# Kernel optimization log

Measured on AMD Instinct MI355X. Metric: run time of the kernel, lower is better.

## Reference

```python
import jax, jax.numpy as jnp
import numpy as np

H = 16
ATTN_TEMP = 1.5
CLS_TEMP = 2.0


def setup_inputs() -> dict:
    key = jax.random.key(0)
    ks = jax.random.split(key, 11)
    B, Nq, Nk, C = 2, 2048, 2048, 1024
    x_q = jax.random.normal(ks[0], (B, Nq, C), jnp.float32)
    x_kv = jax.random.normal(ks[1], (B, Nk, C), jnp.float32)
    cls_token = jax.random.normal(ks[2], (B, 1, C), jnp.float32)
    s = 0.02
    Wq = jax.random.normal(ks[3], (C, C), jnp.float32) * s
    bq = jax.random.normal(ks[4], (C,), jnp.float32) * s
    Wk = jax.random.normal(ks[5], (C, C), jnp.float32) * s
    bk = jax.random.normal(ks[6], (C,), jnp.float32) * s
    Wv = jax.random.normal(ks[7], (C, C), jnp.float32) * s
    bv = jax.random.normal(ks[8], (C,), jnp.float32) * s
    Wp = jax.random.normal(ks[9], (C, C), jnp.float32) * s
    bp = jax.random.normal(ks[10], (C,), jnp.float32) * s
    return {"x_q": x_q, "x_kv": x_kv, "cls_token": cls_token,
            "Wq": Wq, "bq": bq, "Wk": Wk, "bk": bk, "Wv": Wv, "bv": bv,
            "Wp": Wp, "bp": bp}


def reference(x_q, x_kv, cls_token, Wq, bq, Wk, bk, Wv, bv, Wp, bp):
    B, Nq, C = x_q.shape
    Nk = x_kv.shape[1]
    Dh = C // H
    scale = Dh ** -0.5
    # torch Linear: y = x @ W.T + b, W is [out, in]
    q = (x_q @ Wq.T + bq).reshape(B, Nq, H, Dh).transpose(0, 2, 1, 3)   # [B,H,Nq,Dh]
    k = (x_kv @ Wk.T + bk).reshape(B, Nk, H, Dh).transpose(0, 2, 1, 3)  # [B,H,Nk,Dh]
    v = (x_kv @ Wv.T + bv).reshape(B, Nk, H, Dh).transpose(0, 2, 1, 3)  # [B,H,Nk,Dh]
    attn_logits = jnp.einsum('bhqd,bhkd->bhqk', q, k) * (scale / ATTN_TEMP)
    # cls-token affinity mask: raw cls_token (NOT passed through q-proj)
    cls_tok = cls_token.reshape(B, 1, H, Dh).transpose(0, 2, 1, 3)      # [B,H,1,Dh]
    aff = jax.nn.sigmoid(jnp.einsum('bhqd,bhkd->bhqk', cls_tok, k) * (scale / CLS_TEMP))
    aff = aff.mean(axis=1, keepdims=True)                               # [B,1,1,Nk]
    m = aff.min(axis=-1, keepdims=True)
    M = aff.max(axis=-1, keepdims=True)
    aff_mask = (aff - m) / (M - m + 1e-6)
    attn = jax.nn.softmax(attn_logits, axis=-1) * aff_mask              # [B,H,Nq,Nk]
    x = jnp.einsum('bhqk,bhkd->bqhd', attn, v).reshape(B, Nq, C)
    x = x @ Wp.T + bp
    return (x, attn_logits.sum(axis=1) / H, aff_mask)
```

## Files before the change

kernel.cpp:

```cpp
#include <hip/hip_runtime.h>
#include <stdint.h>
#include <math.h>

typedef unsigned short u16;
typedef __attribute__((ext_vector_type(8))) short bh8;
typedef __attribute__((ext_vector_type(4))) float f32x4;
typedef __attribute__((ext_vector_type(16))) float f32x16;

#define MFMA16(a,b,c) __builtin_amdgcn_mfma_f32_16x16x32_bf16((a),(b),(c),0,0,0)
#define MFMA32(a,b,c) __builtin_amdgcn_mfma_f32_32x32x16_bf16((a),(b),(c),0,0,0)

__device__ __forceinline__ int swz3(int r){ return (r ^ (r >> 3)) & 7; }

__device__ __forceinline__ u16 f2bf(float f){
  union { float f; uint32_t i; } x; x.f = f;
  uint32_t r = x.i + 0x7fffu + ((x.i >> 16) & 1u);
  return (u16)(r >> 16);
}
__device__ __forceinline__ float bf2f(u16 u){
  union { uint32_t i; float f; } x; x.i = ((uint32_t)u) << 16; return x.f;
}
__device__ __forceinline__ uint32_t cvtpk(float a, float b){
  uint32_t r;
  asm("v_cvt_pk_bf16_f32 %0, %1, %2" : "=v"(r) : "v"(a), "v"(b));
  return r;
}

__device__ __forceinline__ void gld16(void* lds, const void* g){
  __builtin_amdgcn_global_load_lds(
      (__attribute__((address_space(1))) unsigned int*)const_cast<void*>(g),
      (__attribute__((address_space(3))) unsigned int*)lds, 16, 0, 0);
}

__global__ __launch_bounds__(256) void cvt_all_kernel(
    const float* __restrict__ xq, const float* __restrict__ xkv,
    const float* __restrict__ Wq, const float* __restrict__ Wk,
    const float* __restrict__ Wv, const float* __restrict__ Wp,
    u16* __restrict__ oxq, u16* __restrict__ oxkv,
    u16* __restrict__ oWq, u16* __restrict__ oWk,
    u16* __restrict__ oWv, u16* __restrict__ oWp,
    int nx8, int nw8)
{
  int i = blockIdx.x * 256 + threadIdx.x;
  const float* s; u16* d; int o;
  if (i < 2 * nx8){
    if (i < nx8){ s = xq; d = oxq; o = i; }
    else        { s = xkv; d = oxkv; o = i - nx8; }
  } else {
    int k = i - 2 * nx8;
    if (k >= 4 * nw8) return;
    int wsel = k / nw8; o = k - wsel * nw8;
    s = (wsel == 0) ? Wq : (wsel == 1) ? Wk : (wsel == 2) ? Wv : Wp;
    d = (wsel == 0) ? oWq : (wsel == 1) ? oWk : (wsel == 2) ? oWv : oWp;
  }
  const float4* sp = (const float4*)s + 2 * (size_t)o;
  float4 a = sp[0], b = sp[1];
  bh8 r;
  r[0]=(short)f2bf(a.x); r[1]=(short)f2bf(a.y); r[2]=(short)f2bf(a.z); r[3]=(short)f2bf(a.w);
  r[4]=(short)f2bf(b.x); r[5]=(short)f2bf(b.y); r[6]=(short)f2bf(b.z); r[7]=(short)f2bf(b.w);
  *(bh8*)(d + (size_t)o * 8) = r;
}

template<bool OUT_BF16, bool HAS_BIAS>
__device__ __forceinline__ void gemm_body(
    const u16* __restrict__ A, const u16* __restrict__ Bm,
    const float* __restrict__ bias, void* __restrict__ outp,
    int N, int K, int bm, int bn, float scale,
    u16* As, u16* Bs)
{
  const int tid = threadIdx.x, lane = tid & 63, w = tid >> 6;
  const int wm = w >> 1, wn = w & 1;
  const int l15 = lane & 15, l4 = lane >> 4;
  f32x4 acc[4][4];
  const f32x4 vz = {0.f, 0.f, 0.f, 0.f};
  #pragma unroll
  for (int m = 0; m < 4; ++m)
    #pragma unroll
    for (int n = 0; n < 4; ++n) acc[m][n] = vz;

  const u16* Arow = A + (size_t)bm * K;
  const u16* Brow = Bm + (size_t)bn * K;
  const int nkt = K >> 6;
  for (int kt = 0; kt < nkt; ++kt){
    #pragma unroll
    for (int it = 0; it < 4; ++it){
      int cb = w * 256 + it * 64;
      int c = cb + lane;
      int j = c >> 3;
      int dd = (c & 7) ^ swz3(j);
      gld16(&As[cb * 8], Arow + (size_t)j * K + kt * 64 + dd * 8);
      gld16(&Bs[cb * 8], Brow + (size_t)j * K + kt * 64 + dd * 8);
    }
    __syncthreads();
    #pragma unroll
    for (int s = 0; s < 2; ++s){
      bh8 af[4], bfr[4];
      #pragma unroll
      for (int m = 0; m < 4; ++m){
        int row = wm * 64 + m * 16 + l15;
        af[m] = *(const bh8*)&As[row * 64 + (((s * 4 + l4) ^ swz3(row)) << 3)];
      }
      #pragma unroll
      for (int n = 0; n < 4; ++n){
        int row = wn * 64 + n * 16 + l15;
        bfr[n] = *(const bh8*)&Bs[row * 64 + (((s * 4 + l4) ^ swz3(row)) << 3)];
      }
      #pragma unroll
      for (int m = 0; m < 4; ++m)
        #pragma unroll
        for (int n = 0; n < 4; ++n)
          acc[m][n] = MFMA16(af[m], bfr[n], acc[m][n]);
    }
    __syncthreads();
  }
  #pragma unroll
  for (int m = 0; m < 4; ++m){
    int row0 = bm + wm * 64 + m * 16 + l4 * 4;
    #pragma unroll
    for (int n = 0; n < 4; ++n){
      int col = bn + wn * 64 + n * 16 + l15;
      float bv = HAS_BIAS ? bias[col] : 0.f;
      #pragma unroll
      for (int r = 0; r < 4; ++r){
        float v = (acc[m][n][r] + bv) * scale;
        size_t idx = (size_t)(row0 + r) * N + col;
        if (OUT_BF16) ((u16*)outp)[idx] = f2bf(v);
        else          ((float*)outp)[idx] = v;
      }
    }
  }
}

__global__ __launch_bounds__(256) void proj_gemm_kernel(
    const u16* __restrict__ xq, const u16* __restrict__ xkv,
    const u16* __restrict__ Wq, const u16* __restrict__ Wk, const u16* __restrict__ Wv,
    const float* __restrict__ bq, const float* __restrict__ bk, const float* __restrict__ bv,
    u16* __restrict__ Q, u16* __restrict__ Ko, u16* __restrict__ V, float qscale)
{
  __shared__ __align__(16) u16 As[128 * 64];
  __shared__ __align__(16) u16 Bs[128 * 64];
  int z = blockIdx.z;
  const u16* A   = (z == 0) ? xq : xkv;
  const u16* W   = (z == 0) ? Wq : (z == 1) ? Wk : Wv;
  const float* b = (z == 0) ? bq : (z == 1) ? bk : bv;
  u16* out       = (z == 0) ? Q  : (z == 1) ? Ko : V;
  float sc       = (z == 0) ? qscale : 1.0f;
  gemm_body<true, true>(A, W, b, out, 1024, 1024,
                        blockIdx.y * 128, blockIdx.x * 128, sc, As, Bs);
}

__global__ __launch_bounds__(256) void out1_gemm_kernel(
    const u16* __restrict__ Q, const u16* __restrict__ Kb,
    float* __restrict__ out1, int Nq, int Nk, float scale)
{
  __shared__ __align__(16) u16 As[128 * 64];
  __shared__ __align__(16) u16 Bs[128 * 64];
  int b = blockIdx.z;
  gemm_body<false, false>(Q + (size_t)b * Nq * 1024, Kb + (size_t)b * Nk * 1024,
                          nullptr, out1 + (size_t)b * Nq * Nk, Nk, 1024,
                          blockIdx.y * 128, blockIdx.x * 128, scale, As, Bs);
}

__global__ __launch_bounds__(256) void out0_gemm_kernel(
    const u16* __restrict__ X, const u16* __restrict__ Wp,
    const float* __restrict__ bp, float* __restrict__ out)
{
  __shared__ __align__(16) u16 As[128 * 64];
  __shared__ __align__(16) u16 Bs[128 * 64];
  gemm_body<false, true>(X, Wp, bp, out, 1024, 1024,
                         blockIdx.y * 128, blockIdx.x * 128, 1.0f, As, Bs);
}

__global__ __launch_bounds__(256) void aff_kernel(
    const float* __restrict__ cls, const u16* __restrict__ Kb,
    float* __restrict__ aff, int Nk)
{
  int lane = threadIdx.x & 63;
  int gw = (blockIdx.x * 256 + threadIdx.x) >> 6;
  int b = gw / Nk, j = gw - b * Nk;
  const u16* kr = Kb + ((size_t)(b * Nk + j)) * 1024;
  const float* c = cls + (size_t)b * 1024;
  float total = 0.f;
  #pragma unroll
  for (int half = 0; half < 2; ++half){
    int d0 = half * 512 + lane * 8;
    bh8 kv = *(const bh8*)(kr + d0);
    float4 ca = *(const float4*)(c + d0);
    float4 cb = *(const float4*)(c + d0 + 4);
    float p = bf2f((u16)kv[0]) * ca.x + bf2f((u16)kv[1]) * ca.y
            + bf2f((u16)kv[2]) * ca.z + bf2f((u16)kv[3]) * ca.w
            + bf2f((u16)kv[4]) * cb.x + bf2f((u16)kv[5]) * cb.y
            + bf2f((u16)kv[6]) * cb.z + bf2f((u16)kv[7]) * cb.w;
    p += __shfl_xor(p, 1); p += __shfl_xor(p, 2); p += __shfl_xor(p, 4);
    float sig = 1.f / (1.f + __expf(-0.0625f * p));
    total += sig;
  }
  total += __shfl_xor(total, 8); total += __shfl_xor(total, 16); total += __shfl_xor(total, 32);
  if (lane == 0) aff[gw] = total * (1.0f / 128.0f);
}

__global__ __launch_bounds__(1024) void affnorm_kernel(
    const float* __restrict__ aff, float* __restrict__ mask,
    float* __restrict__ out2, int Nk)
{
  int b = blockIdx.x, tid = threadIdx.x;
  const float* a = aff + (size_t)b * Nk;
  float mn = 1e30f, mx = -1e30f;
  for (int i = tid; i < Nk; i += 1024){
    float v = a[i]; mn = fminf(mn, v); mx = fmaxf(mx, v);
  }
  #pragma unroll
  for (int off = 1; off < 64; off <<= 1){
    mn = fminf(mn, __shfl_xor(mn, off));
    mx = fmaxf(mx, __shfl_xor(mx, off));
  }
  __shared__ float smn[16], smx[16];
  int wv = tid >> 6;
  if ((tid & 63) == 0){ smn[wv] = mn; smx[wv] = mx; }
  __syncthreads();
  mn = smn[tid & 15]; mx = smx[tid & 15];
  #pragma unroll
  for (int off = 1; off < 16; off <<= 1){
    mn = fminf(mn, __shfl_xor(mn, off));
    mx = fmaxf(mx, __shfl_xor(mx, off));
  }
  float inv = 1.f / ((mx - mn) + 1e-6f);
  for (int i = tid; i < Nk; i += 1024){
    float v = (a[i] - mn) * inv;
    mask[(size_t)b * Nk + i] = v;
    out2[(size_t)b * Nk + i] = v;
  }
}

__global__ __launch_bounds__(256) void vtrans_kernel(
    const u16* __restrict__ Vb, const float* __restrict__ affm,
    u16* __restrict__ Vtg, int Nk)
{
  __shared__ u16 T[64][72];
  int t0 = blockIdx.x * 64, h = blockIdx.y, b = blockIdx.z;
  int tid = threadIdx.x;
  int row = tid & 63, cp = tid >> 6;
  const u16* src = Vb + ((size_t)(b * Nk) + t0 + row) * 1024 + h * 64 + cp * 16;
  *(bh8*)&T[row][cp * 16]     = *(const bh8*)(src);
  *(bh8*)&T[row][cp * 16 + 8] = *(const bh8*)(src + 8);
  __syncthreads();
  int d = tid >> 2, kc = (tid & 3) * 16;
  const float* av = affm + (size_t)b * Nk + t0 + kc;
  u16* dst = Vtg + ((size_t)(b * 16 + h) * 64 + d) * 2048 + t0 + kc;
  bh8 o0, o1;
  #pragma unroll
  for (int j = 0; j < 8; ++j)
    o0[j] = (short)f2bf(bf2f(T[kc + j][d]) * av[j]);
  #pragma unroll
  for (int j = 0; j < 8; ++j)
    o1[j] = (short)f2bf(bf2f(T[kc + 8 + j][d]) * av[8 + j]);
  *(bh8*)dst = o0;
  *(bh8*)(dst + 8) = o1;
}

__global__ __launch_bounds__(256) void flash_kernel(
    const u16* __restrict__ Qb, const u16* __restrict__ Kb, const u16* __restrict__ Vtg,
    u16* __restrict__ xo, int Nq, int Nk, int nqb, int perx)
{
  __shared__ __align__(16) u16 Ks[2][64 * 64];
  __shared__ __align__(16) u16 Vs[2][64 * 64];
  const int tid = threadIdx.x, lane = tid & 63, w = tid >> 6;
  const int l31 = lane & 31, hi = lane >> 5;

  int bid = blockIdx.x;
  int xcd = bid & 7, slot = bid >> 3;
  int g = xcd * perx + slot / nqb;
  int qb = slot - (slot / nqb) * nqb;
  int h = g & 15, b = g >> 4;
  int q0 = qb * 128;

  const u16* Qg = Qb + ((size_t)b * Nq + q0 + w * 32 + l31) * 1024 + h * 64;
  const u16* Kg = Kb + ((size_t)b * Nk) * 1024 + h * 64;
  const u16* Vg = Vtg + ((size_t)(b * 16 + h)) * 64 * 2048;

  bh8 qf[4];
  #pragma unroll
  for (int s = 0; s < 4; ++s)
    qf[s] = *(const bh8*)(Qg + s * 16 + hi * 8);

  float lsum = 0.f;
  f32x16 O0, O1;
  #pragma unroll
  for (int r = 0; r < 16; ++r){ O0[r] = 0.f; O1[r] = 0.f; }

  const int nt = Nk >> 6;

  #define STAGE(T, PB) do {                                                    \
    int t_ = (T);                                                              \
    _Pragma("unroll")                                                          \
    for (int it = 0; it < 2; ++it){                                            \
      int cb = (w * 2 + it) * 64;                                              \
      int c = cb + lane;                                                       \
      int j = c >> 3, dd = (c & 7) ^ swz3(j);                                  \
      gld16(&Ks[PB][cb * 8], Kg + (size_t)(t_ * 64 + j) * 1024 + dd * 8);      \
      gld16(&Vs[PB][cb * 8], Vg + (size_t)j * 2048 + t_ * 64 + dd * 8);        \
    }                                                                          \
  } while (0)

  STAGE(0, 0);
  __syncthreads();

  for (int t = 0; t < nt; ++t){
    int pb = t & 1;
    if (t + 1 < nt) STAGE(t + 1, pb ^ 1);

    f32x16 S0, S1;
    #pragma unroll
    for (int s = 0; s < 4; ++s){
      bh8 kf0 = *(const bh8*)&Ks[pb][l31 * 64 + (((s * 2 + hi) ^ swz3(l31)) << 3)];
      bh8 kf1 = *(const bh8*)&Ks[pb][(32 + l31) * 64 + (((s * 2 + hi) ^ swz3(32 + l31)) << 3)];
      if (s == 0){
        f32x16 z;
        #pragma unroll
        for (int r = 0; r < 16; ++r) z[r] = 0.f;
        S0 = MFMA32(kf0, qf[0], z);
        S1 = MFMA32(kf1, qf[0], z);
      } else {
        S0 = MFMA32(kf0, qf[s], S0);
        S1 = MFMA32(kf1, qf[s], S1);
      }
    }

    #pragma unroll
    for (int r = 0; r < 16; ++r) S0[r] = exp2f(S0[r]);
    #pragma unroll
    for (int r = 0; r < 16; ++r) S1[r] = exp2f(S1[r]);
    float rs = 0.f;
    #pragma unroll
    for (int r = 0; r < 16; ++r) rs += S0[r];
    #pragma unroll
    for (int r = 0; r < 16; ++r) rs += S1[r];
    rs += __shfl_xor(rs, 32);
    lsum += rs;

    bh8 pa[4];
    #pragma unroll
    for (int ks = 0; ks < 4; ++ks){
      int r0 = (ks & 1) * 8;
      float p0, p1, p2, p3, p4, p5, p6, p7;
      if (ks < 2){ p0=S0[r0]; p1=S0[r0+1]; p2=S0[r0+2]; p3=S0[r0+3];
                   p4=S0[r0+4]; p5=S0[r0+5]; p6=S0[r0+6]; p7=S0[r0+7]; }
      else       { p0=S1[r0]; p1=S1[r0+1]; p2=S1[r0+2]; p3=S1[r0+3];
                   p4=S1[r0+4]; p5=S1[r0+5]; p6=S1[r0+6]; p7=S1[r0+7]; }
      uint32_t x0 = cvtpk(p0, p1), x1 = cvtpk(p2, p3);
      uint32_t y0 = cvtpk(p4, p5), y1 = cvtpk(p6, p7);
      asm volatile("v_permlane32_swap_b32 %0, %1" : "+v"(x0), "+v"(y0));
      asm volatile("v_permlane32_swap_b32 %0, %1" : "+v"(x1), "+v"(y1));
      union { uint32_t u[4]; bh8 v; } pk;
      pk.u[0] = x0; pk.u[1] = x1; pk.u[2] = y0; pk.u[3] = y1;
      pa[ks] = pk.v;
    }

    #pragma unroll
    for (int ks = 0; ks < 4; ++ks){
      bh8 vf0 = *(const bh8*)&Vs[pb][l31 * 64 + (((ks * 2 + hi) ^ swz3(l31)) << 3)];
      bh8 vf1 = *(const bh8*)&Vs[pb][(32 + l31) * 64 + (((ks * 2 + hi) ^ swz3(32 + l31)) << 3)];
      O0 = MFMA32(pa[ks], vf0, O0);
      O1 = MFMA32(pa[ks], vf1, O1);
    }
    __syncthreads();
  }
  #undef STAGE

  float inv = 1.0f / lsum;
  int hb = hi << 4;
  #pragma unroll
  for (int r = 0; r < 16; ++r){
    int qc = (r & 3) + 8 * (r >> 2);
    float invq = __int_as_float(__builtin_amdgcn_ds_bpermute(qc * 4 + hb, __float_as_int(inv)));
    int qrow = q0 + w * 32 + qc + 4 * hi;
    size_t base = ((size_t)b * Nq + qrow) * 1024 + h * 64;
    xo[base + l31]      = f2bf(O0[r] * invq);
    xo[base + 32 + l31] = f2bf(O1[r] * invq);
  }
}

extern "C" void kernel_launch(void* const* d_in, const int* in_sizes, int n_in,
                              void* d_out, int out_size, void* d_ws, size_t ws_size,
                              hipStream_t stream)
{
  const float* x_q  = (const float*)d_in[0];
  const float* x_kv = (const float*)d_in[1];
  const float* cls  = (const float*)d_in[2];
  const float* bq   = (const float*)d_in[4];
  const float* bk   = (const float*)d_in[6];
  const float* bv   = (const float*)d_in[8];
  const float* bp   = (const float*)d_in[10];
  const float* Wq   = (const float*)d_in[3];
  const float* Wk   = (const float*)d_in[5];
  const float* Wv   = (const float*)d_in[7];
  const float* Wp   = (const float*)d_in[9];

  const int Nq = 2048, Nk = 2048, C = 1024;
  const int B = in_sizes[0] / (Nq * C);
  const size_t nX = (size_t)B * Nq * C;
  const size_t nW = (size_t)C * C;

  char* wsb = (char*)d_ws;
  size_t off = 0;
  auto alloc = [&](size_t bytes) -> char* {
    char* p = wsb + off; off += (bytes + 255) & ~(size_t)255; return p;
  };
  u16* xqb  = (u16*)alloc(nX * 2);
  u16* xkvb = (u16*)alloc(nX * 2);
  u16* Wqb  = (u16*)alloc(nW * 2);
  u16* Wkb  = (u16*)alloc(nW * 2);
  u16* Wvb  = (u16*)alloc(nW * 2);
  u16* Wpb  = (u16*)alloc(nW * 2);
  u16* Qb   = (u16*)alloc(nX * 2);
  u16* Kb   = (u16*)alloc(nX * 2);
  u16* Vb   = (u16*)alloc(nX * 2);
  u16* Vtg  = (u16*)alloc(nX * 2);
  u16* Xat  = (u16*)alloc(nX * 2);
  float* aff  = (float*)alloc((size_t)B * Nk * 4);
  float* affm = (float*)alloc((size_t)B * Nk * 4);

  float* out0 = (float*)d_out;
  float* out1 = out0 + (size_t)B * Nq * C;
  float* out2 = out1 + (size_t)B * Nq * Nk;

  int nx8 = (int)(nX / 8), nw8 = (int)(nW / 8);
  int total = 2 * nx8 + 4 * nw8;
  cvt_all_kernel<<<(total + 255) / 256, 256, 0, stream>>>(
      x_q, x_kv, Wq, Wk, Wv, Wp, xqb, xkvb, Wqb, Wkb, Wvb, Wpb, nx8, nw8);

  const float c2 = (0.125f / 1.5f) * 1.44269504088896f;
  proj_gemm_kernel<<<dim3(C / 128, (B * Nq) / 128, 3), 256, 0, stream>>>(
      xqb, xkvb, Wqb, Wkb, Wvb, bq, bk, bv, Qb, Kb, Vb, c2);

  aff_kernel<<<(B * Nk) / 4, 256, 0, stream>>>(cls, Kb, aff, Nk);
  affnorm_kernel<<<B, 1024, 0, stream>>>(aff, affm, out2, Nk);

  vtrans_kernel<<<dim3(Nk / 64, 16, B), 256, 0, stream>>>(Vb, affm, Vtg, Nk);

  const float c1s = (0.125f / (1.5f * 16.f)) / c2;
  out1_gemm_kernel<<<dim3(Nk / 128, Nq / 128, B), 256, 0, stream>>>(
      Qb, Kb, out1, Nq, Nk, c1s);

  int nqb = Nq / 128;
  int perx = (16 * B) / 8;
  flash_kernel<<<dim3(nqb * 16 * B), 256, 0, stream>>>(
      Qb, Kb, Vtg, Xat, Nq, Nk, nqb, perx);

  out0_gemm_kernel<<<dim3(C / 128, (B * Nq) / 128, 1), 256, 0, stream>>>(
      Xat, Wpb, bp, out0);
}
```

Before: 281.6 us.

## Split flash attention over key halves and merge partials in combine kernel

Splits the flash attention key range into two halves per query block, doubling the grid, and adds a combine kernel that sums the two partial outputs and normalizes by the summed row denominators. The row-sum reduction now runs as an extra MFMA against a ones vector instead of VALU adds plus a shuffle, and exp2f is replaced with a raw v_exp_f32 instruction. It also sets launch_bounds occupancy to 4 and reuses dead workspace buffers for the partials. The goal is more parallelism and less VALU work, at the cost of extra partial-result traffic in bf16 and an additional kernel launch.

```diff
diff --git a/kernel.cpp b/kernel.cpp
--- a/kernel.cpp
+++ b/kernel.cpp
@@ -24,6 +24,9 @@
   uint32_t r;
   asm("v_cvt_pk_bf16_f32 %0, %1, %2" : "=v"(r) : "v"(a), "v"(b));
   return r;
+}
+__device__ __forceinline__ float fexp2(float x){
+  float r; asm("v_exp_f32 %0, %1" : "=v"(r) : "v"(x)); return r;
 }
 
 __device__ __forceinline__ void gld16(void* lds, const void* g){
@@ -258,9 +261,9 @@
   *(bh8*)(dst + 8) = o1;
 }
 
-__global__ __launch_bounds__(256) void flash_kernel(
+__global__ __launch_bounds__(256, 4) void flash_kernel(
     const u16* __restrict__ Qb, const u16* __restrict__ Kb, const u16* __restrict__ Vtg,
-    u16* __restrict__ xo, int Nq, int Nk, int nqb, int perx)
+    u16* __restrict__ Opart, float* __restrict__ Lpart, int Nq, int Nk, int nqb, int perx)
 {
   __shared__ __align__(16) u16 Ks[2][64 * 64];
   __shared__ __align__(16) u16 Vs[2][64 * 64];
@@ -269,26 +272,37 @@
 
   int bid = blockIdx.x;
   int xcd = bid & 7, slot = bid >> 3;
-  int g = xcd * perx + slot / nqb;
-  int qb = slot - (slot / nqb) * nqb;
+  int spg = nqb * 2;
+  int gl = slot / spg;
+  int within = slot - gl * spg;
+  int g = xcd * perx + gl;
+  int qb = within >> 1, sp = within & 1;
   int h = g & 15, b = g >> 4;
   int q0 = qb * 128;
 
   const u16* Qg = Qb + ((size_t)b * Nq + q0 + w * 32 + l31) * 1024 + h * 64;
   const u16* Kg = Kb + ((size_t)b * Nk) * 1024 + h * 64;
-  const u16* Vg = Vtg + ((size_t)(b * 16 + h)) * 64 * 2048;
+  const u16* Vg = Vtg + ((size_t)(b * 16 + h)) * 64 * (size_t)Nk;
 
   bh8 qf[4];
   #pragma unroll
   for (int s = 0; s < 4; ++s)
     qf[s] = *(const bh8*)(Qg + s * 16 + hi * 8);
 
-  float lsum = 0.f;
-  f32x16 O0, O1;
-  #pragma unroll
-  for (int r = 0; r < 16; ++r){ O0[r] = 0.f; O1[r] = 0.f; }
-
-  const int nt = Nk >> 6;
+  union { short s[8]; bh8 v; } one8;
+  #pragma unroll
+  for (int j = 0; j < 8; ++j) one8.s[j] = (short)0x3F80;
+  const bh8 onesf = one8.v;
+
+  f32x16 O0, O1, Lacc;
+  #pragma unroll
+  for (int r = 0; r < 16; ++r){ O0[r] = 0.f; O1[r] = 0.f; Lacc[r] = 0.f; }
+  f32x16 z16;
+  #pragma unroll
+  for (int r = 0; r < 16; ++r) z16[r] = 0.f;
+
+  const int tpers = (Nk >> 6) >> 1;
+  const int t0 = sp * tpers;
 
   #define STAGE(T, PB) do {                                                    \
     int t_ = (T);                                                              \
@@ -298,16 +312,16 @@
       int c = cb + lane;                                                       \
       int j = c >> 3, dd = (c & 7) ^ swz3(j);                                  \
       gld16(&Ks[PB][cb * 8], Kg + (size_t)(t_ * 64 + j) * 1024 + dd * 8);      \
-      gld16(&Vs[PB][cb * 8], Vg + (size_t)j * 2048 + t_ * 64 + dd * 8);        \
+      gld16(&Vs[PB][cb * 8], Vg + (size_t)j * Nk + t_ * 64 + dd * 8);          \
     }                                                                          \
   } while (0)
 
-  STAGE(0, 0);
+  STAGE(t0, 0);
   __syncthreads();
 
-  for (int t = 0; t < nt; ++t){
-    int pb = t & 1;
-    if (t + 1 < nt) STAGE(t + 1, pb ^ 1);
+  for (int ti = 0; ti < tpers; ++ti){
+    int pb = ti & 1;
+    if (ti + 1 < tpers) STAGE(t0 + ti + 1, pb ^ 1);
 
     f32x16 S0, S1;
     #pragma unroll
@@ -315,11 +329,8 @@
       bh8 kf0 = *(const bh8*)&Ks[pb][l31 * 64 + (((s * 2 + hi) ^ swz3(l31)) << 3)];
       bh8 kf1 = *(const bh8*)&Ks[pb][(32 + l31) * 64 + (((s * 2 + hi) ^ swz3(32 + l31)) << 3)];
       if (s == 0){
-        f32x16 z;
-        #pragma unroll
-        for (int r = 0; r < 16; ++r) z[r] = 0.f;
-        S0 = MFMA32(kf0, qf[0], z);
-        S1 = MFMA32(kf1, qf[0], z);
+        S0 = MFMA32(kf0, qf[0], z16);
+        S1 = MFMA32(kf1, qf[0], z16);
       } else {
         S0 = MFMA32(kf0, qf[s], S0);
         S1 = MFMA32(kf1, qf[s], S1);
@@ -327,16 +338,9 @@
     }
 
     #pragma unroll
-    for (int r = 0; r < 16; ++r) S0[r] = exp2f(S0[r]);
-    #pragma unroll
-    for (int r = 0; r < 16; ++r) S1[r] = exp2f(S1[r]);
-    float rs = 0.f;
-    #pragma unroll
-    for (int r = 0; r < 16; ++r) rs += S0[r];
-    #pragma unroll
-    for (int r = 0; r < 16; ++r) rs += S1[r];
-    rs += __shfl_xor(rs, 32);
-    lsum += rs;
+    for (int r = 0; r < 16; ++r) S0[r] = fexp2(S0[r]);
+    #pragma unroll
+    for (int r = 0; r < 16; ++r) S1[r] = fexp2(S1[r]);
 
     bh8 pa[4];
     #pragma unroll
@@ -362,22 +366,46 @@
       bh8 vf1 = *(const bh8*)&Vs[pb][(32 + l31) * 64 + (((ks * 2 + hi) ^ swz3(32 + l31)) << 3)];
       O0 = MFMA32(pa[ks], vf0, O0);
       O1 = MFMA32(pa[ks], vf1, O1);
+      Lacc = MFMA32(pa[ks], onesf, Lacc);
     }
     __syncthreads();
   }
   #undef STAGE
 
-  float inv = 1.0f / lsum;
-  int hb = hi << 4;
+  size_t gs = (size_t)(g * 2 + sp);
   #pragma unroll
   for (int r = 0; r < 16; ++r){
     int qc = (r & 3) + 8 * (r >> 2);
-    float invq = __int_as_float(__builtin_amdgcn_ds_bpermute(qc * 4 + hb, __float_as_int(inv)));
     int qrow = q0 + w * 32 + qc + 4 * hi;
-    size_t base = ((size_t)b * Nq + qrow) * 1024 + h * 64;
-    xo[base + l31]      = f2bf(O0[r] * invq);
-    xo[base + 32 + l31] = f2bf(O1[r] * invq);
-  }
+    size_t base = (gs * Nq + qrow) * 64;
+    Opart[base + l31]      = f2bf(O0[r]);
+    Opart[base + 32 + l31] = f2bf(O1[r]);
+    if (l31 == 0) Lpart[gs * Nq + qrow] = Lacc[r];
+  }
+}
+
+__global__ __launch_bounds__(256) void combine_kernel(
+    const u16* __restrict__ Opart, const float* __restrict__ Lpart,
+    u16* __restrict__ xo, int Nq)
+{
+  int i = blockIdx.x * 256 + threadIdx.x;
+  int g = i >> 14;
+  int rem = i & 16383;
+  int q = rem >> 3, dc = (rem & 7) << 3;
+  size_t ba = (((size_t)g * 2 + 0) * Nq + q) * 64 + dc;
+  size_t bb = (((size_t)g * 2 + 1) * Nq + q) * 64 + dc;
+  float la = Lpart[((size_t)g * 2 + 0) * Nq + q];
+  float lb = Lpart[((size_t)g * 2 + 1) * Nq + q];
+  float inv = 1.f / (la + lb);
+  bh8 av = *(const bh8*)(Opart + ba);
+  bh8 bv = *(const bh8*)(Opart + bb);
+  int b_ = g >> 4, h = g & 15;
+  u16* dst = xo + ((size_t)b_ * Nq + q) * 1024 + h * 64 + dc;
+  bh8 o;
+  #pragma unroll
+  for (int j = 0; j < 8; ++j)
+    o[j] = (short)f2bf((bf2f((u16)av[j]) + bf2f((u16)bv[j])) * inv);
+  *(bh8*)dst = o;
 }
 
 extern "C" void kernel_launch(void* const* d_in, const int* in_sizes, int n_in,
@@ -417,8 +445,10 @@
   u16* Vb   = (u16*)alloc(nX * 2);
   u16* Vtg  = (u16*)alloc(nX * 2);
   u16* Xat  = (u16*)alloc(nX * 2);
-  float* aff  = (float*)alloc((size_t)B * Nk * 4);
-  float* affm = (float*)alloc((size_t)B * Nk * 4);
+  float* aff   = (float*)alloc((size_t)B * Nk * 4);
+  float* affm  = (float*)alloc((size_t)B * Nk * 4);
+  u16*   Opart = xqb;
+  float* Lpart = (float*)Wqb;
 
   float* out0 = (float*)d_out;
   float* out1 = out0 + (size_t)B * Nq * C;
@@ -444,8 +474,10 @@
 
   int nqb = Nq / 128;
   int perx = (16 * B) / 8;
-  flash_kernel<<<dim3(nqb * 16 * B), 256, 0, stream>>>(
-      Qb, Kb, Vtg, Xat, Nq, Nk, nqb, perx);
+  flash_kernel<<<dim3(nqb * 16 * B * 2), 256, 0, stream>>>(
+      Qb, Kb, Vtg, Opart, Lpart, Nq, Nk, nqb, perx);
+
+  combine_kernel<<<(16 * B * Nq * 8) / 256, 256, 0, stream>>>(Opart, Lpart, Xat, Nq);
 
   out0_gemm_kernel<<<dim3(C / 128, (B * Nq) / 128, 1), 256, 0, stream>>>(
       Xat, Wpb, bp, out0);
```

New measurement: 269.4 us. 1.05x faster.
